# Performance work log

Measured on AMD Instinct MI355X. Metric: run time of the kernel, lower is better.

Reference implementation:

```python
import jax, jax.numpy as jnp
import numpy as np

TEMPERATURE = 0.1


def setup_inputs() -> dict:
    key = jax.random.key(0)
    k1, k2 = jax.random.split(key)
    N, D = 4096, 128
    return {
        "anchor_embeddings": jax.random.normal(k1, (N, D), dtype=jnp.float32),
        "target_embeddings": jax.random.normal(k2, (N, D), dtype=jnp.float32),
    }


def _l2_normalize(x, axis=-1, eps=1e-12):
    # matches tf.math.l2_normalize
    sq = jnp.sum(x * x, axis=axis, keepdims=True)
    return x * jax.lax.rsqrt(jnp.maximum(sq, eps))


def reference(anchor_embeddings, target_embeddings):
    N = anchor_embeddings.shape[0]
    # l2-normalize both views; cosine_similarity of unit vectors == dot product,
    # so the original's broadcasted (2N,2N,D) product + internal re-normalization
    # reduces to a single [2N,D] @ [D,2N] matmul.
    a = _l2_normalize(anchor_embeddings, axis=1)
    t = _l2_normalize(target_embeddings, axis=1)
    z = jnp.concatenate([a, t], axis=0)              # [2N, D]
    sim = jnp.einsum("id,jd->ij", z, z)              # [2N, 2N]

    # positives: diag_part(k=+N) and diag_part(k=-N)
    sim_ij = jnp.diagonal(sim, offset=N)             # [N]
    sim_ji = jnp.diagonal(sim, offset=-N)            # [N]
    positives = jnp.concatenate([sim_ij, sim_ji], axis=0)  # [2N]

    logits = sim / TEMPERATURE                       # [2N, 2N]
    # negative_mask = ~eye(2N): exclude self-similarity from the denominator
    diag_mask = jnp.eye(2 * N, dtype=bool)
    denom = jnp.sum(jnp.where(diag_mask, 0.0, jnp.exp(logits)), axis=1)  # [2N]

    loss_partial = -(positives / TEMPERATURE - jnp.log(denom))           # [2N]
    loss = jnp.sum(loss_partial) / (2 * N)
    return loss
```

## Files before the change

kernel.cpp:

```cpp
#include <hip/hip_runtime.h>

#define N_ROWS 4096
#define TN 8192
#define DIM 128
#define LOG2E10 14.426950408889634f

#define Z_BYTE_OFF 36864

typedef __attribute__((ext_vector_type(8))) short short8;
typedef __attribute__((ext_vector_type(4))) float f32x4;

static __device__ __forceinline__ ushort f2bf(float f) {
    union { float f; unsigned u; } a; a.f = f;
    unsigned r = a.u + 0x7FFF + ((a.u >> 16) & 1);
    return (ushort)(r >> 16);
}

__global__ __launch_bounds__(256) void prep_kernel(
    const float* __restrict__ anchor, const float* __restrict__ target,
    ushort* __restrict__ z, float* __restrict__ pos_accum)
{
    int wave = threadIdx.x >> 6;
    int lane = threadIdx.x & 63;
    int i    = blockIdx.x * 4 + wave;
    float2 a = ((const float2*)(anchor + (size_t)i * DIM))[lane];
    float2 t = ((const float2*)(target + (size_t)i * DIM))[lane];
    float sa = a.x * a.x + a.y * a.y;
    float st = t.x * t.x + t.y * t.y;
    float dt = a.x * t.x + a.y * t.y;
    #pragma unroll
    for (int m = 1; m < 64; m <<= 1) {
        sa += __shfl_xor(sa, m, 64);
        st += __shfl_xor(st, m, 64);
        dt += __shfl_xor(dt, m, 64);
    }
    float rsa = rsqrtf(fmaxf(sa, 1e-12f));
    float rst = rsqrtf(fmaxf(st, 1e-12f));
    ushort2 za, zt;
    za.x = f2bf(a.x * rsa); za.y = f2bf(a.y * rsa);
    zt.x = f2bf(t.x * rst); zt.y = f2bf(t.y * rst);
    ((ushort2*)(z + (size_t)i * DIM))[lane] = za;
    ((ushort2*)(z + (size_t)(i + N_ROWS) * DIM))[lane] = zt;
    __shared__ float red[4];
    if (lane == 0) red[wave] = dt * rsa * rst;
    __syncthreads();
    if (threadIdx.x == 0)
        atomicAdd(pos_accum, red[0] + red[1] + red[2] + red[3]);
}

__global__ __launch_bounds__(256) void simgemm_kernel(
    const ushort* __restrict__ z, float* __restrict__ denom)
{
    int wave = threadIdx.x >> 6;
    int lane = threadIdx.x & 63;
    int r = lane & 15;
    int g = lane >> 4;
    int wr = wave >> 1, wc = wave & 1;
    int rowbase = blockIdx.x * 128 + wr * 64;
    int wcol    = blockIdx.y * 1024 + wc * 512;

    short8 a[4][4];
    #pragma unroll
    for (int rt = 0; rt < 4; ++rt)
        #pragma unroll
        for (int kt = 0; kt < 4; ++kt)
            a[rt][kt] = *(const short8*)(z + (size_t)(rowbase + rt * 16 + r) * DIM
                                           + kt * 32 + g * 8);

    float ps[4][4];
    #pragma unroll
    for (int rt = 0; rt < 4; ++rt)
        #pragma unroll
        for (int q = 0; q < 4; ++q) ps[rt][q] = 0.0f;

    bool wavediag = ((unsigned)(rowbase - wcol) < 512u);

    const ushort* pb = z + (size_t)(wcol + r) * DIM + g * 8;

#define LOADB(buf, ptr)                                \
    {   buf[0] = *(const short8*)(ptr);                \
        buf[1] = *(const short8*)((ptr) + 32);         \
        buf[2] = *(const short8*)((ptr) + 64);         \
        buf[3] = *(const short8*)((ptr) + 96); }

#define COMPUTE(ct, b)                                                        \
    {   int c0 = wcol + (ct) * 16;                                            \
        bool dtile = wavediag && ((unsigned)(c0 - rowbase) < 64u);            \
        if (!dtile) {                                                         \
            _Pragma("unroll")                                                 \
            for (int rt = 0; rt < 4; ++rt) {                                  \
                f32x4 acc = {0.f, 0.f, 0.f, 0.f};                             \
                _Pragma("unroll")                                             \
                for (int kt = 0; kt < 4; ++kt)                                \
                    acc = __builtin_amdgcn_mfma_f32_16x16x32_bf16(            \
                        a[rt][kt], b[kt], acc, 0, 0, 0);                      \
                _Pragma("unroll")                                             \
                for (int q = 0; q < 4; ++q)                                   \
                    ps[rt][q] += exp2f(acc[q] * LOG2E10);                     \
            }                                                                 \
        } else {                                                              \
            int gcol = c0 + r;                                                \
            _Pragma("unroll")                                                 \
            for (int rt = 0; rt < 4; ++rt) {                                  \
                f32x4 acc = {0.f, 0.f, 0.f, 0.f};                             \
                _Pragma("unroll")                                             \
                for (int kt = 0; kt < 4; ++kt)                                \
                    acc = __builtin_amdgcn_mfma_f32_16x16x32_bf16(            \
                        a[rt][kt], b[kt], acc, 0, 0, 0);                      \
                _Pragma("unroll")                                             \
                for (int q = 0; q < 4; ++q) {                                 \
                    float e = exp2f(acc[q] * LOG2E10);                        \
                    int grow = rowbase + rt * 16 + g * 4 + q;                 \
                    ps[rt][q] += (grow == gcol) ? 0.0f : e;                   \
                }                                                             \
            }                                                                 \
        } }

    short8 b0[4], b1[4];
    LOADB(b0, pb);
    for (int ct = 0; ct < 32; ct += 2) {
        const ushort* pn = pb + (ct + 1) * (16 * DIM);
        LOADB(b1, pn);
        COMPUTE(ct, b0);
        if (ct + 2 < 32) {
            const ushort* pn2 = pb + (ct + 2) * (16 * DIM);
            LOADB(b0, pn2);
        }
        COMPUTE(ct + 1, b1);
    }
#undef LOADB
#undef COMPUTE

    #pragma unroll
    for (int rt = 0; rt < 4; ++rt)
        #pragma unroll
        for (int q = 0; q < 4; ++q) {
            float v = ps[rt][q];
            v += __shfl_xor(v, 1, 64);
            v += __shfl_xor(v, 2, 64);
            v += __shfl_xor(v, 4, 64);
            v += __shfl_xor(v, 8, 64);
            if (r == 0)
                atomicAdd(&denom[rowbase + rt * 16 + g * 4 + q], v);
        }
}

__global__ __launch_bounds__(1024) void finalize_kernel(
    const float* __restrict__ denom, const float* __restrict__ pos_accum,
    float* __restrict__ out)
{
    int tid = threadIdx.x;
    float s = 0.0f;
    #pragma unroll
    for (int u = 0; u < TN / 1024; ++u) s += logf(denom[u * 1024 + tid]);
    #pragma unroll
    for (int m = 1; m < 64; m <<= 1) s += __shfl_xor(s, m, 64);
    __shared__ float red[16];
    if ((tid & 63) == 0) red[tid >> 6] = s;
    __syncthreads();
    if (tid == 0) {
        float tot = 0.0f;
        #pragma unroll
        for (int i = 0; i < 16; ++i) tot += red[i];
        out[0] = (tot - 20.0f * pos_accum[0]) / (float)TN;
    }
}

extern "C" void kernel_launch(void* const* d_in, const int* in_sizes, int n_in,
                              void* d_out, int out_size, void* d_ws, size_t ws_size,
                              hipStream_t stream) {
    const float* anchor = (const float*)d_in[0];
    const float* target = (const float*)d_in[1];
    float* denom     = (float*)d_ws;
    float* pos_accum = denom + TN;
    ushort* z        = (ushort*)((char*)d_ws + Z_BYTE_OFF);

    hipMemsetAsync(d_ws, 0, (TN + 8) * sizeof(float), stream);
    prep_kernel<<<N_ROWS / 4, 256, 0, stream>>>(anchor, target, z, pos_accum);
    simgemm_kernel<<<dim3(TN / 128, 8), 256, 0, stream>>>(z, denom);
    finalize_kernel<<<1, 1024, 0, stream>>>(denom, pos_accum, (float*)d_out);
}
```

Before: 113.5 us.

## Fold exp2 scale into normalized embeddings, split column tiles, drop positive atomics

Each normalized row is scaled by sqrt(log2(e)/T) before the bf16 cast, so the dot product already sits in base-2 logit units and the per-element multiply plus library exp2f become a bare hardware exp2. The GEMM grid doubles along columns with half the column span per wave, and a launch-bounds occupancy hint is added, to put more blocks in flight. The positive sum now writes per-block partials that finalize reduces, replacing a global atomic and shrinking the memset. The scaled values (magnitude about 3.8) are rounded to bf16, which adds quantization error to the logits, and the extra column split means more denominator atomics.

```diff
diff --git a/kernel.cpp b/kernel.cpp
--- a/kernel.cpp
+++ b/kernel.cpp
@@ -3,7 +3,7 @@
 #define N_ROWS 4096
 #define TN 8192
 #define DIM 128
-#define LOG2E10 14.426950408889634f
+#define SQRT_C 3.79828266f
 
 #define Z_BYTE_OFF 36864
 
@@ -18,7 +18,7 @@
 
 __global__ __launch_bounds__(256) void prep_kernel(
     const float* __restrict__ anchor, const float* __restrict__ target,
-    ushort* __restrict__ z, float* __restrict__ pos_accum)
+    ushort* __restrict__ z, float* __restrict__ pos_part)
 {
     int wave = threadIdx.x >> 6;
     int lane = threadIdx.x & 63;
@@ -34,21 +34,22 @@
         st += __shfl_xor(st, m, 64);
         dt += __shfl_xor(dt, m, 64);
     }
-    float rsa = rsqrtf(fmaxf(sa, 1e-12f));
+    float rsa = rsqrtf(fmaxf(sa, 1e-12f)) ;
     float rst = rsqrtf(fmaxf(st, 1e-12f));
+    float ka = rsa * SQRT_C, kt = rst * SQRT_C;
     ushort2 za, zt;
-    za.x = f2bf(a.x * rsa); za.y = f2bf(a.y * rsa);
-    zt.x = f2bf(t.x * rst); zt.y = f2bf(t.y * rst);
+    za.x = f2bf(a.x * ka); za.y = f2bf(a.y * ka);
+    zt.x = f2bf(t.x * kt); zt.y = f2bf(t.y * kt);
     ((ushort2*)(z + (size_t)i * DIM))[lane] = za;
     ((ushort2*)(z + (size_t)(i + N_ROWS) * DIM))[lane] = zt;
     __shared__ float red[4];
     if (lane == 0) red[wave] = dt * rsa * rst;
     __syncthreads();
     if (threadIdx.x == 0)
-        atomicAdd(pos_accum, red[0] + red[1] + red[2] + red[3]);
+        pos_part[blockIdx.x] = red[0] + red[1] + red[2] + red[3];
 }
 
-__global__ __launch_bounds__(256) void simgemm_kernel(
+__global__ __launch_bounds__(256, 4) void simgemm_kernel(
     const ushort* __restrict__ z, float* __restrict__ denom)
 {
     int wave = threadIdx.x >> 6;
@@ -57,7 +58,7 @@
     int g = lane >> 4;
     int wr = wave >> 1, wc = wave & 1;
     int rowbase = blockIdx.x * 128 + wr * 64;
-    int wcol    = blockIdx.y * 1024 + wc * 512;
+    int wcol    = blockIdx.y * 512 + wc * 256;
 
     short8 a[4][4];
     #pragma unroll
@@ -73,7 +74,7 @@
         #pragma unroll
         for (int q = 0; q < 4; ++q) ps[rt][q] = 0.0f;
 
-    bool wavediag = ((unsigned)(rowbase - wcol) < 512u);
+    bool wavediag = ((unsigned)(rowbase - wcol) < 256u);
 
     const ushort* pb = z + (size_t)(wcol + r) * DIM + g * 8;
 
@@ -96,7 +97,7 @@
                         a[rt][kt], b[kt], acc, 0, 0, 0);                      \
                 _Pragma("unroll")                                             \
                 for (int q = 0; q < 4; ++q)                                   \
-                    ps[rt][q] += exp2f(acc[q] * LOG2E10);                     \
+                    ps[rt][q] += __builtin_amdgcn_exp2f(acc[q]);              \
             }                                                                 \
         } else {                                                              \
             int gcol = c0 + r;                                                \
@@ -109,7 +110,7 @@
                         a[rt][kt], b[kt], acc, 0, 0, 0);                      \
                 _Pragma("unroll")                                             \
                 for (int q = 0; q < 4; ++q) {                                 \
-                    float e = exp2f(acc[q] * LOG2E10);                        \
+                    float e = __builtin_amdgcn_exp2f(acc[q]);                 \
                     int grow = rowbase + rt * 16 + g * 4 + q;                 \
                     ps[rt][q] += (grow == gcol) ? 0.0f : e;                   \
                 }                                                             \
@@ -118,11 +119,11 @@
 
     short8 b0[4], b1[4];
     LOADB(b0, pb);
-    for (int ct = 0; ct < 32; ct += 2) {
+    for (int ct = 0; ct < 16; ct += 2) {
         const ushort* pn = pb + (ct + 1) * (16 * DIM);
         LOADB(b1, pn);
         COMPUTE(ct, b0);
-        if (ct + 2 < 32) {
+        if (ct + 2 < 16) {
             const ushort* pn2 = pb + (ct + 2) * (16 * DIM);
             LOADB(b0, pn2);
         }
@@ -146,23 +147,27 @@
 }
 
 __global__ __launch_bounds__(1024) void finalize_kernel(
-    const float* __restrict__ denom, const float* __restrict__ pos_accum,
+    const float* __restrict__ denom, const float* __restrict__ pos_part,
     float* __restrict__ out)
 {
     int tid = threadIdx.x;
-    float s = 0.0f;
+    float slog = 0.0f;
     #pragma unroll
-    for (int u = 0; u < TN / 1024; ++u) s += logf(denom[u * 1024 + tid]);
+    for (int u = 0; u < TN / 1024; ++u) slog += logf(denom[u * 1024 + tid]);
+    float spos = pos_part[tid];
     #pragma unroll
-    for (int m = 1; m < 64; m <<= 1) s += __shfl_xor(s, m, 64);
-    __shared__ float red[16];
-    if ((tid & 63) == 0) red[tid >> 6] = s;
+    for (int m = 1; m < 64; m <<= 1) {
+        slog += __shfl_xor(slog, m, 64);
+        spos += __shfl_xor(spos, m, 64);
+    }
+    __shared__ float redl[16], redp[16];
+    if ((tid & 63) == 0) { redl[tid >> 6] = slog; redp[tid >> 6] = spos; }
     __syncthreads();
     if (tid == 0) {
-        float tot = 0.0f;
+        float tl = 0.0f, tp = 0.0f;
         #pragma unroll
-        for (int i = 0; i < 16; ++i) tot += red[i];
-        out[0] = (tot - 20.0f * pos_accum[0]) / (float)TN;
+        for (int i = 0; i < 16; ++i) { tl += redl[i]; tp += redp[i]; }
+        out[0] = (tl - 20.0f * tp) / (float)TN;
     }
 }
 
@@ -171,12 +176,12 @@
                               hipStream_t stream) {
     const float* anchor = (const float*)d_in[0];
     const float* target = (const float*)d_in[1];
-    float* denom     = (float*)d_ws;
-    float* pos_accum = denom + TN;
-    ushort* z        = (ushort*)((char*)d_ws + Z_BYTE_OFF);
+    float* denom    = (float*)d_ws;
+    float* pos_part = denom + TN;
+    ushort* z       = (ushort*)((char*)d_ws + Z_BYTE_OFF);
 
-    hipMemsetAsync(d_ws, 0, (TN + 8) * sizeof(float), stream);
-    prep_kernel<<<N_ROWS / 4, 256, 0, stream>>>(anchor, target, z, pos_accum);
-    simgemm_kernel<<<dim3(TN / 128, 8), 256, 0, stream>>>(z, denom);
-    finalize_kernel<<<1, 1024, 0, stream>>>(denom, pos_accum, (float*)d_out);
+    hipMemsetAsync(d_ws, 0, TN * sizeof(float), stream);
+    prep_kernel<<<N_ROWS / 4, 256, 0, stream>>>(anchor, target, z, pos_part);
+    simgemm_kernel<<<dim3(TN / 128, 16), 256, 0, stream>>>(z, denom);
+    finalize_kernel<<<1, 1024, 0, stream>>>(denom, pos_part, (float*)d_out);
 }
```

New measurement: 148.5 us. 30.9% more time.
